# Kernel optimization log

Hardware: AMD Instinct MI355X
Metric: run time of the kernel (lower is better)

## Reference

```python
import jax, jax.numpy as jnp
import numpy as np

B, N_R, N_H, RD, HD = 128, 1, 63, 9, 5
N = N_R + N_H
X_DIM = 128
HID = 64  # wr/wh hidden width
NEG_SLOPE = 0.04
MASK_VAL = -9.0e15


def _glorot(key, shape):
    fan_in, fan_out = shape[0], shape[1]
    lim = jnp.sqrt(6.0 / (fan_in + fan_out))
    return jax.random.uniform(key, shape, jnp.float32, -lim, lim)


def setup_inputs() -> dict:
    key = jax.random.key(0)
    ks = jax.random.split(key, 16)
    d = {
        "robot_state": jax.random.normal(ks[0], (B, N_R, RD), jnp.float32),
        "human_states": jax.random.normal(ks[1], (B, N_H, HD), jnp.float32),
        # w_r: Linear(9->64) ReLU Linear(64->128) ReLU
        "wr_W1": _glorot(ks[2], (RD, HID)), "wr_b1": jnp.zeros((HID,), jnp.float32),
        "wr_W2": _glorot(ks[3], (HID, X_DIM)), "wr_b2": jnp.zeros((X_DIM,), jnp.float32),
        # w_h: Linear(5->64) ReLU Linear(64->128) ReLU
        "wh_W1": _glorot(ks[4], (HD, HID)), "wh_b1": jnp.zeros((HID,), jnp.float32),
        "wh_W2": _glorot(ks[5], (HID, X_DIM)), "wh_b2": jnp.zeros((X_DIM,), jnp.float32),
        # gat0.w_a: Linear(256->256) ReLU Linear(256->1)
        "g0_W1": _glorot(ks[6], (2 * X_DIM, 2 * X_DIM)), "g0_b1": jnp.zeros((2 * X_DIM,), jnp.float32),
        "g0_W2": _glorot(ks[7], (2 * X_DIM, 1)), "g0_b2": jnp.zeros((1,), jnp.float32),
        # gat1.w_a
        "g1_W1": _glorot(ks[8], (2 * X_DIM, 2 * X_DIM)), "g1_b1": jnp.zeros((2 * X_DIM,), jnp.float32),
        "g1_W2": _glorot(ks[9], (2 * X_DIM, 1)), "g1_b2": jnp.zeros((1,), jnp.float32),
    }
    return d


def _mlp2(x, W1, b1, W2, b2, last_relu):
    h = jax.nn.relu(x @ W1 + b1)
    y = h @ W2 + b2
    return jax.nn.relu(y) if last_relu else y


def _gat_layer(X, adj, W1, b1, W2, b2):
    # X: [B, N, D]; pairwise features [B, N, N, 2D] (row i = source, col j = target)
    b, n, d = X.shape
    Pi = jnp.broadcast_to(X[:, :, None, :], (b, n, n, d))
    Pj = jnp.broadcast_to(X[:, None, :, :], (b, n, n, d))
    pair = jnp.concatenate([Pi, Pj], axis=-1)            # [B,N,N,2D]
    A = _mlp2(pair, W1, b1, W2, b2, last_relu=False)[..., 0]  # [B,N,N]
    e = jnp.where(A > 0, A, NEG_SLOPE * A)               # LeakyReLU(0.04)
    masked = jnp.where(adj > 0, e, MASK_VAL)
    attn = jax.nn.softmax(masked, axis=2)
    return jnp.matmul(attn, X)                            # [B,N,D]


def reference(robot_state, human_states,
              wr_W1, wr_b1, wr_W2, wr_b2,
              wh_W1, wh_b1, wh_W2, wh_b2,
              g0_W1, g0_b1, g0_W2, g0_b2,
              g1_W1, g1_b1, g1_W2, g1_b2):
    # adjacency: all-ones except humans cannot attend to robot (col 0)
    adj = jnp.ones((N, N), jnp.float32).at[N_R:, 0].set(0.0)
    adj = jnp.broadcast_to(adj, (robot_state.shape[0], N, N))
    r_emb = _mlp2(robot_state, wr_W1, wr_b1, wr_W2, wr_b2, last_relu=True)
    h_emb = _mlp2(human_states, wh_W1, wh_b1, wh_W2, wh_b2, last_relu=True)
    X = jnp.concatenate([r_emb, h_emb], axis=1)           # [B,N,X_DIM]
    H1 = _gat_layer(X, adj, g0_W1, g0_b1, g0_W2, g0_b2)
    H2 = _gat_layer(H1, adj, g1_W1, g1_b1, g1_W2, g1_b2)
    return H1 + H2 + X  # skip_connection=True
```

## Files before the change

kernel.cpp:

```cpp
#include <hip/hip_runtime.h>

#define NEG_SLOPE 0.04f
#define MASK_VAL  -9.0e15f

namespace {
constexpr int Bz = 128;
constexpr int NN = 64;
constexpr int XD = 128;
constexpr int HID = 64;
}

__device__ __forceinline__ void gat_layer(
    const float* __restrict__ Ns, float* __restrict__ Vs, float* __restrict__ UsAs,
    const float* __restrict__ W1, const float* __restrict__ b1,
    const float* __restrict__ W2, const float* __restrict__ b2,
    int h, int t, float4& o0, float4& o1)
{
  const int w = t >> 6, l = t & 63;

  {
    float vac[8][4];
#pragma unroll
    for (int nn = 0; nn < 8; ++nn)
#pragma unroll
      for (int c = 0; c < 4; ++c) vac[nn][c] = 0.f;

    for (int ks = 0; ks < XD; ks += 4) {
      float wr[4][4];
#pragma unroll
      for (int kk = 0; kk < 4; ++kk) {
        const float4 wv = *reinterpret_cast<const float4*>(&W1[(XD + ks + kk) * 256 + (l << 2)]);
        wr[kk][0] = wv.x; wr[kk][1] = wv.y; wr[kk][2] = wv.z; wr[kk][3] = wv.w;
      }
#pragma unroll
      for (int nn = 0; nn < 8; ++nn) {
        const float4 x4 = *reinterpret_cast<const float4*>(&Ns[(8 * w + nn) * XD + ks]);
        const float xk0 = x4.x, xk1 = x4.y, xk2 = x4.z, xk3 = x4.w;
#pragma unroll
        for (int c = 0; c < 4; ++c) {
          vac[nn][c] = fmaf(xk0, wr[0][c], vac[nn][c]);
          vac[nn][c] = fmaf(xk1, wr[1][c], vac[nn][c]);
          vac[nn][c] = fmaf(xk2, wr[2][c], vac[nn][c]);
          vac[nn][c] = fmaf(xk3, wr[3][c], vac[nn][c]);
        }
      }
    }
#pragma unroll
    for (int nn = 0; nn < 8; ++nn) {
      const int n = 8 * w + nn;
      const float4 v = {vac[nn][0], vac[nn][1], vac[nn][2], vac[nn][3]};
      *reinterpret_cast<float4*>(&Vs[n * 256 + ((l ^ (n & 7)) << 2)]) = v;
    }
  }

  {
    float uac[4][4];
    const float4 bi = *reinterpret_cast<const float4*>(&b1[l << 2]);
#pragma unroll
    for (int q = 0; q < 4; ++q) { uac[q][0] = bi.x; uac[q][1] = bi.y; uac[q][2] = bi.z; uac[q][3] = bi.w; }

    for (int ks = 0; ks < XD; ks += 4) {
      float wr[4][4];
#pragma unroll
      for (int kk = 0; kk < 4; ++kk) {
        const float4 wv = *reinterpret_cast<const float4*>(&W1[(ks + kk) * 256 + (l << 2)]);
        wr[kk][0] = wv.x; wr[kk][1] = wv.y; wr[kk][2] = wv.z; wr[kk][3] = wv.w;
      }
#pragma unroll
      for (int q = 0; q < 4; ++q) {
        const float4 x4 = *reinterpret_cast<const float4*>(&Ns[(32 * h + 4 * w + q) * XD + ks]);
        const float xk0 = x4.x, xk1 = x4.y, xk2 = x4.z, xk3 = x4.w;
#pragma unroll
        for (int c = 0; c < 4; ++c) {
          uac[q][c] = fmaf(xk0, wr[0][c], uac[q][c]);
          uac[q][c] = fmaf(xk1, wr[1][c], uac[q][c]);
          uac[q][c] = fmaf(xk2, wr[2][c], uac[q][c]);
          uac[q][c] = fmaf(xk3, wr[3][c], uac[q][c]);
        }
      }
    }
#pragma unroll
    for (int q = 0; q < 4; ++q) {
      const float4 u = {uac[q][0], uac[q][1], uac[q][2], uac[q][3]};
      *reinterpret_cast<float4*>(&UsAs[(4 * w + q) * 256 + (l << 2)]) = u;
    }
  }
  __syncthreads();

  float att[4];
  {
    const int jx = l & 7;
    float e[4] = {0.f, 0.f, 0.f, 0.f};
    for (int c4 = 0; c4 < 64; ++c4) {
      const float4 v4 = *reinterpret_cast<const float4*>(&Vs[l * 256 + ((c4 ^ jx) << 2)]);
      const float4 w4 = *reinterpret_cast<const float4*>(&W2[c4 << 2]);
#pragma unroll
      for (int q = 0; q < 4; ++q) {
        const float4 u4 = *reinterpret_cast<const float4*>(&UsAs[(4 * w + q) * 256 + (c4 << 2)]);
        e[q] = fmaf(fmaxf(u4.x + v4.x, 0.f), w4.x, e[q]);
        e[q] = fmaf(fmaxf(u4.y + v4.y, 0.f), w4.y, e[q]);
        e[q] = fmaf(fmaxf(u4.z + v4.z, 0.f), w4.z, e[q]);
        e[q] = fmaf(fmaxf(u4.w + v4.w, 0.f), w4.w, e[q]);
      }
    }
    const float bias2 = b2[0];
#pragma unroll
    for (int q = 0; q < 4; ++q) {
      float s = e[q] + bias2;
      s = s > 0.f ? s : NEG_SLOPE * s;
      const int gi = 32 * h + 4 * w + q;
      if (gi > 0 && l == 0) s = MASK_VAL;
      float m = s;
#pragma unroll
      for (int off = 32; off > 0; off >>= 1) m = fmaxf(m, __shfl_xor(m, off));
      const float p = __expf(s - m);
      float sum = p;
#pragma unroll
      for (int off = 32; off > 0; off >>= 1) sum += __shfl_xor(sum, off);
      att[q] = p / sum;
    }
  }
  __syncthreads();
#pragma unroll
  for (int q = 0; q < 4; ++q) UsAs[(4 * w + q) * 64 + l] = att[q];
  __syncthreads();

  {
    const int grp = t >> 5, d4 = (t & 31) << 2;
    float4 a0 = {0.f, 0.f, 0.f, 0.f}, a1 = {0.f, 0.f, 0.f, 0.f};
    for (int j = 0; j < NN; ++j) {
      const float4 x4 = *reinterpret_cast<const float4*>(&Ns[j * XD + d4]);
      const float wA = UsAs[grp * 64 + j];
      const float wB = UsAs[(grp + 16) * 64 + j];
      a0.x = fmaf(wA, x4.x, a0.x); a0.y = fmaf(wA, x4.y, a0.y);
      a0.z = fmaf(wA, x4.z, a0.z); a0.w = fmaf(wA, x4.w, a0.w);
      a1.x = fmaf(wB, x4.x, a1.x); a1.y = fmaf(wB, x4.y, a1.y);
      a1.z = fmaf(wB, x4.z, a1.z); a1.w = fmaf(wB, x4.w, a1.w);
    }
    o0 = a0; o1 = a1;
  }
}

__global__ __launch_bounds__(512) void layer1_kernel(
    const float* __restrict__ robot, const float* __restrict__ human,
    const float* __restrict__ wrW1, const float* __restrict__ wrb1,
    const float* __restrict__ wrW2, const float* __restrict__ wrb2,
    const float* __restrict__ whW1, const float* __restrict__ whb1,
    const float* __restrict__ whW2, const float* __restrict__ whb2,
    const float* __restrict__ W1, const float* __restrict__ b1,
    const float* __restrict__ W2, const float* __restrict__ b2,
    float* __restrict__ Xg, float* __restrict__ H1g)
{
  __shared__ float smem[32768];
  float* Xs = smem;
  float* Vs = smem + 8192;
  float* Us = smem + 24576;
  float* hs = smem + 24576;

  const int b = blockIdx.x >> 1, h = blockIdx.x & 1;
  const int t = threadIdx.x;

  for (int v = t; v < NN * HID; v += 512) {
    const int n = v >> 6, k = v & 63;
    float acc;
    if (n == 0) {
      acc = wrb1[k];
      for (int j = 0; j < 9; ++j) acc = fmaf(robot[b * 9 + j], wrW1[j * HID + k], acc);
    } else {
      const float* in = human + (b * 63 + n - 1) * 5;
      acc = whb1[k];
      for (int j = 0; j < 5; ++j) acc = fmaf(in[j], whW1[j * HID + k], acc);
    }
    hs[v] = fmaxf(acc, 0.f);
  }
  __syncthreads();

  {
    const int d = t & 127, which = t >> 7;
    float xacc[16];
#pragma unroll
    for (int c = 0; c < 16; ++c) xacc[c] = whb2[d];

    for (int k4 = 0; k4 < 16; ++k4) {
      float w4[4];
#pragma unroll
      for (int kk = 0; kk < 4; ++kk) w4[kk] = whW2[(4 * k4 + kk) * XD + d];
#pragma unroll
      for (int c = 0; c < 16; ++c) {
        const float4 h4 = *reinterpret_cast<const float4*>(&hs[(4 * c + which) * HID + 4 * k4]);
        xacc[c] = fmaf(h4.x, w4[0], xacc[c]);
        xacc[c] = fmaf(h4.y, w4[1], xacc[c]);
        xacc[c] = fmaf(h4.z, w4[2], xacc[c]);
        xacc[c] = fmaf(h4.w, w4[3], xacc[c]);
      }
    }
    if (which == 0) {
      float a = wrb2[d];
#pragma unroll 8
      for (int k = 0; k < HID; ++k) a = fmaf(hs[k], wrW2[k * XD + d], a);
      xacc[0] = a;
    }
#pragma unroll
    for (int c = 0; c < 16; ++c) {
      const int n = 4 * c + which;
      const float val = fmaxf(xacc[c], 0.f);
      Xs[n * XD + d] = val;
      if ((n >> 5) == h) Xg[((size_t)(b * NN + n)) * XD + d] = val;
    }
  }
  __syncthreads();

  float4 a0, a1;
  gat_layer(Xs, Vs, Us, W1, b1, W2, b2, h, t, a0, a1);

  const int grp = t >> 5, d4 = (t & 31) << 2;
  const int n0 = 32 * h + grp, n1 = n0 + 16;
  *reinterpret_cast<float4*>(&H1g[((size_t)(b * NN + n0)) * XD + d4]) = a0;
  *reinterpret_cast<float4*>(&H1g[((size_t)(b * NN + n1)) * XD + d4]) = a1;
}

__global__ __launch_bounds__(512) void layer2_kernel(
    const float* __restrict__ H1g, const float* __restrict__ Xg,
    const float* __restrict__ W1, const float* __restrict__ b1,
    const float* __restrict__ W2, const float* __restrict__ b2,
    float* __restrict__ out)
{
  __shared__ float smem[32768];
  float* Ys = smem;
  float* Vs = smem + 8192;
  float* Us = smem + 24576;

  const int b = blockIdx.x >> 1, h = blockIdx.x & 1;
  const int t = threadIdx.x;

  const float* Hb = H1g + (size_t)b * NN * XD;
  for (int idx = t; idx < NN * XD / 4; idx += 512)
    *reinterpret_cast<float4*>(Ys + idx * 4) =
        *reinterpret_cast<const float4*>(Hb + idx * 4);
  __syncthreads();

  float4 a0, a1;
  gat_layer(Ys, Vs, Us, W1, b1, W2, b2, h, t, a0, a1);

  const int grp = t >> 5, d4 = (t & 31) << 2;
  const int n0 = 32 * h + grp, n1 = n0 + 16;
  const float4 y0 = *reinterpret_cast<const float4*>(&Ys[n0 * XD + d4]);
  const float4 y1 = *reinterpret_cast<const float4*>(&Ys[n1 * XD + d4]);
  const float4 x0 = *reinterpret_cast<const float4*>(&Xg[((size_t)(b * NN + n0)) * XD + d4]);
  const float4 x1 = *reinterpret_cast<const float4*>(&Xg[((size_t)(b * NN + n1)) * XD + d4]);
  a0.x += y0.x + x0.x; a0.y += y0.y + x0.y; a0.z += y0.z + x0.z; a0.w += y0.w + x0.w;
  a1.x += y1.x + x1.x; a1.y += y1.y + x1.y; a1.z += y1.z + x1.z; a1.w += y1.w + x1.w;
  *reinterpret_cast<float4*>(&out[((size_t)(b * NN + n0)) * XD + d4]) = a0;
  *reinterpret_cast<float4*>(&out[((size_t)(b * NN + n1)) * XD + d4]) = a1;
}

extern "C" void kernel_launch(void* const* d_in, const int* in_sizes, int n_in,
                              void* d_out, int out_size, void* d_ws, size_t ws_size,
                              hipStream_t stream) {
  const float* robot = (const float*)d_in[0];
  const float* human = (const float*)d_in[1];
  const float* wrW1  = (const float*)d_in[2];
  const float* wrb1  = (const float*)d_in[3];
  const float* wrW2  = (const float*)d_in[4];
  const float* wrb2  = (const float*)d_in[5];
  const float* whW1  = (const float*)d_in[6];
  const float* whb1  = (const float*)d_in[7];
  const float* whW2  = (const float*)d_in[8];
  const float* whb2  = (const float*)d_in[9];
  const float* g0W1  = (const float*)d_in[10];
  const float* g0b1  = (const float*)d_in[11];
  const float* g0W2  = (const float*)d_in[12];
  const float* g0b2  = (const float*)d_in[13];
  const float* g1W1  = (const float*)d_in[14];
  const float* g1b1  = (const float*)d_in[15];
  const float* g1W2  = (const float*)d_in[16];
  const float* g1b2  = (const float*)d_in[17];
  float* out = (float*)d_out;

  float* Xg  = (float*)d_ws;
  float* H1g = Xg + (size_t)Bz * NN * XD;

  layer1_kernel<<<Bz * 2, 512, 0, stream>>>(robot, human, wrW1, wrb1, wrW2, wrb2,
                                            whW1, whb1, whW2, whb2,
                                            g0W1, g0b1, g0W2, g0b2, Xg, H1g);
  layer2_kernel<<<Bz * 2, 512, 0, stream>>>(H1g, Xg, g1W1, g1b1, g1W2, g1b2, out);
}
```

Measured before the change: 174.1 us.

## Chunk GAT hidden dimension into 64-wide slices to shrink shared memory

The GAT layer now computes the V and U projections in four 64-column chunks of the 256-wide hidden dimension and accumulates the attention logits per chunk, instead of materialising the full 64x256 V and 32x256 U tiles. This cuts shared memory from 128KB to about 56KB per block, and launch bounds now request 4 blocks per CU, so more blocks should fit on a CU for better occupancy. The cost is three extra barriers per chunk loop and a new thread mapping (16 column groups, each covering two V rows and one U row). That mapping changes the W1 access pattern and may raise register pressure under the tighter launch bound.

Measured after the change: 279.0 us. 1.6x slower.

```diff
diff --git a/kernel.cpp b/kernel.cpp
--- a/kernel.cpp
+++ b/kernel.cpp
@@ -2,6 +2,10 @@
 
 #define NEG_SLOPE 0.04f
 #define MASK_VAL  -9.0e15f
+
+#define FMA4(acc, s, w4) \
+  acc.x = fmaf(s, w4.x, acc.x); acc.y = fmaf(s, w4.y, acc.y); \
+  acc.z = fmaf(s, w4.z, acc.z); acc.w = fmaf(s, w4.w, acc.w)
 
 namespace {
 constexpr int Bz = 128;
@@ -11,137 +15,99 @@
 }
 
 __device__ __forceinline__ void gat_layer(
-    const float* __restrict__ Ns, float* __restrict__ Vs, float* __restrict__ UsAs,
+    const float* __restrict__ Ns, float* __restrict__ VU, float* __restrict__ UsAs,
     const float* __restrict__ W1, const float* __restrict__ b1,
     const float* __restrict__ W2, const float* __restrict__ b2,
     int h, int t, float4& o0, float4& o1)
 {
-  const int w = t >> 6, l = t & 63;
-
-  {
-    float vac[8][4];
-#pragma unroll
-    for (int nn = 0; nn < 8; ++nn)
-#pragma unroll
-      for (int c = 0; c < 4; ++c) vac[nn][c] = 0.f;
-
+  const int w  = t >> 6, l = t & 63;
+  const int cq = t & 15;
+  const int g  = t >> 4;
+  const int n0 = 2 * g;
+  const int jx = l & 15;
+
+  float e[4] = {0.f, 0.f, 0.f, 0.f};
+
+  for (int cb = 0; cb < 4; ++cb) {
+    const int c0 = cb * 64 + 4 * cq;
+    float4 v0a = {0.f,0.f,0.f,0.f}, v1a = {0.f,0.f,0.f,0.f};
+    float4 ua  = *reinterpret_cast<const float4*>(&b1[c0]);
+    const float* x0p = &Ns[n0 * XD];
+    const float* x1p = &Ns[(n0 + 1) * XD];
+    const float* xrp = &Ns[(32 * h + g) * XD];
+#pragma unroll 2
     for (int ks = 0; ks < XD; ks += 4) {
-      float wr[4][4];
-#pragma unroll
-      for (int kk = 0; kk < 4; ++kk) {
-        const float4 wv = *reinterpret_cast<const float4*>(&W1[(XD + ks + kk) * 256 + (l << 2)]);
-        wr[kk][0] = wv.x; wr[kk][1] = wv.y; wr[kk][2] = wv.z; wr[kk][3] = wv.w;
-      }
-#pragma unroll
-      for (int nn = 0; nn < 8; ++nn) {
-        const float4 x4 = *reinterpret_cast<const float4*>(&Ns[(8 * w + nn) * XD + ks]);
-        const float xk0 = x4.x, xk1 = x4.y, xk2 = x4.z, xk3 = x4.w;
-#pragma unroll
-        for (int c = 0; c < 4; ++c) {
-          vac[nn][c] = fmaf(xk0, wr[0][c], vac[nn][c]);
-          vac[nn][c] = fmaf(xk1, wr[1][c], vac[nn][c]);
-          vac[nn][c] = fmaf(xk2, wr[2][c], vac[nn][c]);
-          vac[nn][c] = fmaf(xk3, wr[3][c], vac[nn][c]);
-        }
-      }
-    }
-#pragma unroll
-    for (int nn = 0; nn < 8; ++nn) {
-      const int n = 8 * w + nn;
-      const float4 v = {vac[nn][0], vac[nn][1], vac[nn][2], vac[nn][3]};
-      *reinterpret_cast<float4*>(&Vs[n * 256 + ((l ^ (n & 7)) << 2)]) = v;
-    }
-  }
-
-  {
-    float uac[4][4];
-    const float4 bi = *reinterpret_cast<const float4*>(&b1[l << 2]);
-#pragma unroll
-    for (int q = 0; q < 4; ++q) { uac[q][0] = bi.x; uac[q][1] = bi.y; uac[q][2] = bi.z; uac[q][3] = bi.w; }
-
-    for (int ks = 0; ks < XD; ks += 4) {
-      float wr[4][4];
-#pragma unroll
-      for (int kk = 0; kk < 4; ++kk) {
-        const float4 wv = *reinterpret_cast<const float4*>(&W1[(ks + kk) * 256 + (l << 2)]);
-        wr[kk][0] = wv.x; wr[kk][1] = wv.y; wr[kk][2] = wv.z; wr[kk][3] = wv.w;
-      }
+      float4 wv0 = *reinterpret_cast<const float4*>(&W1[(XD + ks    ) * 256 + c0]);
+      float4 wv1 = *reinterpret_cast<const float4*>(&W1[(XD + ks + 1) * 256 + c0]);
+      float4 wv2 = *reinterpret_cast<const float4*>(&W1[(XD + ks + 2) * 256 + c0]);
+      float4 wv3 = *reinterpret_cast<const float4*>(&W1[(XD + ks + 3) * 256 + c0]);
+      float4 wu0 = *reinterpret_cast<const float4*>(&W1[(ks    ) * 256 + c0]);
+      float4 wu1 = *reinterpret_cast<const float4*>(&W1[(ks + 1) * 256 + c0]);
+      float4 wu2 = *reinterpret_cast<const float4*>(&W1[(ks + 2) * 256 + c0]);
+      float4 wu3 = *reinterpret_cast<const float4*>(&W1[(ks + 3) * 256 + c0]);
+      const float4 xa = *reinterpret_cast<const float4*>(&x0p[ks]);
+      const float4 xb = *reinterpret_cast<const float4*>(&x1p[ks]);
+      const float4 xc = *reinterpret_cast<const float4*>(&xrp[ks]);
+      FMA4(v0a, xa.x, wv0); FMA4(v0a, xa.y, wv1); FMA4(v0a, xa.z, wv2); FMA4(v0a, xa.w, wv3);
+      FMA4(v1a, xb.x, wv0); FMA4(v1a, xb.y, wv1); FMA4(v1a, xb.z, wv2); FMA4(v1a, xb.w, wv3);
+      FMA4(ua,  xc.x, wu0); FMA4(ua,  xc.y, wu1); FMA4(ua,  xc.z, wu2); FMA4(ua,  xc.w, wu3);
+    }
+    *reinterpret_cast<float4*>(&VU[n0 * 64 + ((cq ^ (n0 & 15)) << 2)])       = v0a;
+    *reinterpret_cast<float4*>(&VU[(n0+1) * 64 + ((cq ^ ((n0+1) & 15)) << 2)]) = v1a;
+    *reinterpret_cast<float4*>(&UsAs[g * 64 + 4 * cq]) = ua;
+    __syncthreads();
+
+    for (int q4 = 0; q4 < 16; ++q4) {
+      const float4 v4 = *reinterpret_cast<const float4*>(&VU[l * 64 + ((q4 ^ jx) << 2)]);
+      const float4 w4 = *reinterpret_cast<const float4*>(&W2[cb * 64 + 4 * q4]);
 #pragma unroll
       for (int q = 0; q < 4; ++q) {
-        const float4 x4 = *reinterpret_cast<const float4*>(&Ns[(32 * h + 4 * w + q) * XD + ks]);
-        const float xk0 = x4.x, xk1 = x4.y, xk2 = x4.z, xk3 = x4.w;
-#pragma unroll
-        for (int c = 0; c < 4; ++c) {
-          uac[q][c] = fmaf(xk0, wr[0][c], uac[q][c]);
-          uac[q][c] = fmaf(xk1, wr[1][c], uac[q][c]);
-          uac[q][c] = fmaf(xk2, wr[2][c], uac[q][c]);
-          uac[q][c] = fmaf(xk3, wr[3][c], uac[q][c]);
-        }
-      }
-    }
-#pragma unroll
-    for (int q = 0; q < 4; ++q) {
-      const float4 u = {uac[q][0], uac[q][1], uac[q][2], uac[q][3]};
-      *reinterpret_cast<float4*>(&UsAs[(4 * w + q) * 256 + (l << 2)]) = u;
-    }
-  }
-  __syncthreads();
-
-  float att[4];
-  {
-    const int jx = l & 7;
-    float e[4] = {0.f, 0.f, 0.f, 0.f};
-    for (int c4 = 0; c4 < 64; ++c4) {
-      const float4 v4 = *reinterpret_cast<const float4*>(&Vs[l * 256 + ((c4 ^ jx) << 2)]);
-      const float4 w4 = *reinterpret_cast<const float4*>(&W2[c4 << 2]);
-#pragma unroll
-      for (int q = 0; q < 4; ++q) {
-        const float4 u4 = *reinterpret_cast<const float4*>(&UsAs[(4 * w + q) * 256 + (c4 << 2)]);
+        const float4 u4 = *reinterpret_cast<const float4*>(&UsAs[(4*w + q) * 64 + 4 * q4]);
         e[q] = fmaf(fmaxf(u4.x + v4.x, 0.f), w4.x, e[q]);
         e[q] = fmaf(fmaxf(u4.y + v4.y, 0.f), w4.y, e[q]);
         e[q] = fmaf(fmaxf(u4.z + v4.z, 0.f), w4.z, e[q]);
         e[q] = fmaf(fmaxf(u4.w + v4.w, 0.f), w4.w, e[q]);
       }
     }
-    const float bias2 = b2[0];
-#pragma unroll
-    for (int q = 0; q < 4; ++q) {
-      float s = e[q] + bias2;
-      s = s > 0.f ? s : NEG_SLOPE * s;
-      const int gi = 32 * h + 4 * w + q;
-      if (gi > 0 && l == 0) s = MASK_VAL;
-      float m = s;
-#pragma unroll
-      for (int off = 32; off > 0; off >>= 1) m = fmaxf(m, __shfl_xor(m, off));
-      const float p = __expf(s - m);
-      float sum = p;
-#pragma unroll
-      for (int off = 32; off > 0; off >>= 1) sum += __shfl_xor(sum, off);
-      att[q] = p / sum;
-    }
-  }
-  __syncthreads();
-#pragma unroll
-  for (int q = 0; q < 4; ++q) UsAs[(4 * w + q) * 64 + l] = att[q];
+    __syncthreads();
+  }
+
+  float att[4];
+  const float bias2 = b2[0];
+#pragma unroll
+  for (int q = 0; q < 4; ++q) {
+    float s = e[q] + bias2;
+    s = s > 0.f ? s : NEG_SLOPE * s;
+    const int gi = 32 * h + 4 * w + q;
+    if (gi > 0 && l == 0) s = MASK_VAL;
+    float m = s;
+#pragma unroll
+    for (int off = 32; off > 0; off >>= 1) m = fmaxf(m, __shfl_xor(m, off));
+    const float p = __expf(s - m);
+    float sum = p;
+#pragma unroll
+    for (int off = 32; off > 0; off >>= 1) sum += __shfl_xor(sum, off);
+    att[q] = p / sum;
+  }
+#pragma unroll
+  for (int q = 0; q < 4; ++q) UsAs[(4*w + q) * 64 + l] = att[q];
   __syncthreads();
 
   {
     const int grp = t >> 5, d4 = (t & 31) << 2;
-    float4 a0 = {0.f, 0.f, 0.f, 0.f}, a1 = {0.f, 0.f, 0.f, 0.f};
+    float4 a0 = {0.f,0.f,0.f,0.f}, a1 = {0.f,0.f,0.f,0.f};
     for (int j = 0; j < NN; ++j) {
       const float4 x4 = *reinterpret_cast<const float4*>(&Ns[j * XD + d4]);
       const float wA = UsAs[grp * 64 + j];
       const float wB = UsAs[(grp + 16) * 64 + j];
-      a0.x = fmaf(wA, x4.x, a0.x); a0.y = fmaf(wA, x4.y, a0.y);
-      a0.z = fmaf(wA, x4.z, a0.z); a0.w = fmaf(wA, x4.w, a0.w);
-      a1.x = fmaf(wB, x4.x, a1.x); a1.y = fmaf(wB, x4.y, a1.y);
-      a1.z = fmaf(wB, x4.z, a1.z); a1.w = fmaf(wB, x4.w, a1.w);
+      FMA4(a0, wA, x4);
+      FMA4(a1, wB, x4);
     }
     o0 = a0; o1 = a1;
   }
 }
 
-__global__ __launch_bounds__(512) void layer1_kernel(
+__global__ __launch_bounds__(512, 4) void layer1_kernel(
     const float* __restrict__ robot, const float* __restrict__ human,
     const float* __restrict__ wrW1, const float* __restrict__ wrb1,
     const float* __restrict__ wrW2, const float* __restrict__ wrb2,
@@ -151,11 +117,11 @@
     const float* __restrict__ W2, const float* __restrict__ b2,
     float* __restrict__ Xg, float* __restrict__ H1g)
 {
-  __shared__ float smem[32768];
-  float* Xs = smem;
-  float* Vs = smem + 8192;
-  float* Us = smem + 24576;
-  float* hs = smem + 24576;
+  __shared__ float smem[14336];
+  float* Xs   = smem;
+  float* VU   = smem + 8192;
+  float* UsAs = smem + 12288;
+  float* hs   = VU;
 
   const int b = blockIdx.x >> 1, h = blockIdx.x & 1;
   const int t = threadIdx.x;
@@ -211,24 +177,24 @@
   __syncthreads();
 
   float4 a0, a1;
-  gat_layer(Xs, Vs, Us, W1, b1, W2, b2, h, t, a0, a1);
+  gat_layer(Xs, VU, UsAs, W1, b1, W2, b2, h, t, a0, a1);
 
   const int grp = t >> 5, d4 = (t & 31) << 2;
-  const int n0 = 32 * h + grp, n1 = n0 + 16;
-  *reinterpret_cast<float4*>(&H1g[((size_t)(b * NN + n0)) * XD + d4]) = a0;
-  *reinterpret_cast<float4*>(&H1g[((size_t)(b * NN + n1)) * XD + d4]) = a1;
-}
-
-__global__ __launch_bounds__(512) void layer2_kernel(
+  const int nA = 32 * h + grp, nB = nA + 16;
+  *reinterpret_cast<float4*>(&H1g[((size_t)(b * NN + nA)) * XD + d4]) = a0;
+  *reinterpret_cast<float4*>(&H1g[((size_t)(b * NN + nB)) * XD + d4]) = a1;
+}
+
+__global__ __launch_bounds__(512, 4) void layer2_kernel(
     const float* __restrict__ H1g, const float* __restrict__ Xg,
     const float* __restrict__ W1, const float* __restrict__ b1,
     const float* __restrict__ W2, const float* __restrict__ b2,
     float* __restrict__ out)
 {
-  __shared__ float smem[32768];
-  float* Ys = smem;
-  float* Vs = smem + 8192;
-  float* Us = smem + 24576;
+  __shared__ float smem[14336];
+  float* Ys   = smem;
+  float* VU   = smem + 8192;
+  float* UsAs = smem + 12288;
 
   const int b = blockIdx.x >> 1, h = blockIdx.x & 1;
   const int t = threadIdx.x;
@@ -240,18 +206,18 @@
   __syncthreads();
 
   float4 a0, a1;
-  gat_layer(Ys, Vs, Us, W1, b1, W2, b2, h, t, a0, a1);
+  gat_layer(Ys, VU, UsAs, W1, b1, W2, b2, h, t, a0, a1);
 
   const int grp = t >> 5, d4 = (t & 31) << 2;
-  const int n0 = 32 * h + grp, n1 = n0 + 16;
-  const float4 y0 = *reinterpret_cast<const float4*>(&Ys[n0 * XD + d4]);
-  const float4 y1 = *reinterpret_cast<const float4*>(&Ys[n1 * XD + d4]);
-  const float4 x0 = *reinterpret_cast<const float4*>(&Xg[((size_t)(b * NN + n0)) * XD + d4]);
-  const float4 x1 = *reinterpret_cast<const float4*>(&Xg[((size_t)(b * NN + n1)) * XD + d4]);
+  const int nA = 32 * h + grp, nB = nA + 16;
+  const float4 y0 = *reinterpret_cast<const float4*>(&Ys[nA * XD + d4]);
+  const float4 y1 = *reinterpret_cast<const float4*>(&Ys[nB * XD + d4]);
+  const float4 x0 = *reinterpret_cast<const float4*>(&Xg[((size_t)(b * NN + nA)) * XD + d4]);
+  const float4 x1 = *reinterpret_cast<const float4*>(&Xg[((size_t)(b * NN + nB)) * XD + d4]);
   a0.x += y0.x + x0.x; a0.y += y0.y + x0.y; a0.z += y0.z + x0.z; a0.w += y0.w + x0.w;
   a1.x += y1.x + x1.x; a1.y += y1.y + x1.y; a1.z += y1.z + x1.z; a1.w += y1.w + x1.w;
-  *reinterpret_cast<float4*>(&out[((size_t)(b * NN + n0)) * XD + d4]) = a0;
-  *reinterpret_cast<float4*>(&out[((size_t)(b * NN + n1)) * XD + d4]) = a1;
+  *reinterpret_cast<float4*>(&out[((size_t)(b * NN + nA)) * XD + d4]) = a0;
+  *reinterpret_cast<float4*>(&out[((size_t)(b * NN + nB)) * XD + d4]) = a1;
 }
 
 extern "C" void kernel_launch(void* const* d_in, const int* in_sizes, int n_in,
```
